# Performance work log

Hardware: AMD Instinct MI355X
Metric: run time of the kernel (lower is better)

The kernel has to match this reference:

```python
import jax, jax.numpy as jnp
import numpy as np

B = 2048
TT_IN = (16, 16, 16)    # prod = 4096
TT_OUT = (16, 16, 16)   # prod = 4096
BOND = (32, 32)
INIT_STD = 0.05  # keras 'random_normal' default stddev


def setup_inputs() -> dict:
    key = jax.random.key(0)
    k_x, k1, k2, k3 = jax.random.split(key, 4)
    x = jax.random.normal(k_x, (B, int(np.prod(TT_IN))), dtype=jnp.float32)
    core1 = jax.random.normal(k1, (TT_IN[0], TT_OUT[0], BOND[0]), dtype=jnp.float32) * INIT_STD
    core2 = jax.random.normal(k2, (TT_IN[1], TT_OUT[1], BOND[0], BOND[1]), dtype=jnp.float32) * INIT_STD
    core3 = jax.random.normal(k3, (TT_IN[2], TT_OUT[2], BOND[1]), dtype=jnp.float32) * INIT_STD
    bias = jnp.zeros(TT_OUT, dtype=jnp.float32)
    return {"x": x, "core1": core1, "core2": core2, "core3": core3, "bias": bias}


def reference(x, core1, core2, core3, bias):
    # x: [B, 4096] -> [B, x, y, z] tensor-train input modes
    xt = x.reshape((x.shape[0],) + TT_IN)
    # TT contraction: modes x,y,z contracted with cores; a,b,c are output
    # modes; p,q are bond indices (matches original einsum structure for
    # 3 cores: x[1,2,3], c1[1,4,7], c2[2,5,7,8], c3[3,6,8] -> [4,5,6]).
    out = jnp.einsum('nxyz,xap,ybpq,zcq->nabc', xt, core1, core2, core3,
                     optimize='optimal')
    out = out + bias  # bias broadcast over batch, shape TT_OUT
    out = out.reshape(x.shape[0], -1)  # [B, prod(TT_OUT)]
    return jax.nn.relu(out)
```

## Files before the change

kernel.cpp:

```cpp
#include <hip/hip_runtime.h>
#include <hip/hip_bf16.h>
#include <stdint.h>


typedef short bf16x8 __attribute__((ext_vector_type(8)));
typedef float f32x4  __attribute__((ext_vector_type(4)));

#define MB 2048
#define KD 4096
#define ND 4096
#define NT_K 64

__device__ __forceinline__ unsigned short f32_bf16(float f) {
  union { float f; uint32_t u; } v; v.f = f;
  return (unsigned short)((v.u + 0x7fffu + ((v.u >> 16) & 1u)) >> 16);
}
__device__ __forceinline__ float bf2f(unsigned short u) {
  union { uint32_t i; float f; } v; v.i = ((uint32_t)u) << 16; return v.f;
}

__global__ void k_conv(const float* __restrict__ x, unsigned short* __restrict__ xb) {
  int i = blockIdx.x * 256 + threadIdx.x;
  const float4* x4 = (const float4*)x;
  float4 a = x4[2*i];
  float4 b = x4[2*i+1];
  ushort4 lo, hi;
  lo.x = f32_bf16(a.x); lo.y = f32_bf16(a.y); lo.z = f32_bf16(a.z); lo.w = f32_bf16(a.w);
  hi.x = f32_bf16(b.x); hi.y = f32_bf16(b.y); hi.z = f32_bf16(b.z); hi.w = f32_bf16(b.w);
  ushort4* o = (ushort4*)xb;
  o[2*i]   = lo;
  o[2*i+1] = hi;
}

__global__ __launch_bounds__(256) void k_wt(const float* __restrict__ c1,
                                            const float* __restrict__ c2,
                                            const float* __restrict__ c3,
                                            unsigned short* __restrict__ Wt) {
  __shared__ unsigned short sh[17472];
  int ab = blockIdx.x;
  int t = threadIdx.x;
  int a = ab >> 4, b = ab & 15;
  unsigned short* c2s = sh;
  float* c1s = (float*)(sh + 16448);

  #pragma unroll
  for (int y = 0; y < 16; ++y) {
    float4 v = *(const float4*)(c2 + (size_t)(y*16 + b)*1024 + t*4);
    ushort4 s;
    s.x = f32_bf16(v.x); s.y = f32_bf16(v.y); s.z = f32_bf16(v.z); s.w = f32_bf16(v.w);
    *(ushort4*)(c2s + y*1028 + t*4) = s;
  }
  c1s[t]       = c1[((t>>5)*16 + a)*32 + (t&31)];
  c1s[t+256]   = c1[(((t>>5)+8)*16 + a)*32 + (t&31)];
  __syncthreads();

  int xx = t >> 4, yy = t & 15;
  const float* c1r = c1s + xx*32;
  const unsigned short* c2r = c2s + yy*1028;
  float acc[32];
  #pragma unroll
  for (int q = 0; q < 32; ++q) acc[q] = 0.f;
  #pragma unroll 8
  for (int p = 0; p < 32; ++p) {
    float w = c1r[p];
    #pragma unroll
    for (int j = 0; j < 8; ++j) {
      ushort4 v = *(const ushort4*)(c2r + p*32 + j*4);
      acc[4*j+0] = fmaf(w, bf2f(v.x), acc[4*j+0]);
      acc[4*j+1] = fmaf(w, bf2f(v.y), acc[4*j+1]);
      acc[4*j+2] = fmaf(w, bf2f(v.z), acc[4*j+2]);
      acc[4*j+3] = fmaf(w, bf2f(v.w), acc[4*j+3]);
    }
  }
  __syncthreads();

  unsigned short* T2s  = sh;
  unsigned short* c3ps = sh + 8192;

  #pragma unroll
  for (int j = 0; j < 8; ++j) {
    ushort4 s;
    s.x = f32_bf16(acc[4*j+0]); s.y = f32_bf16(acc[4*j+1]);
    s.z = f32_bf16(acc[4*j+2]); s.w = f32_bf16(acc[4*j+3]);
    *(ushort4*)(T2s + t*32 + j*4) = s;
  }
  #pragma unroll
  for (int r = 0; r < 8; ++r) {
    int i4 = t*8 + r;
    float4 v = *(const float4*)(c3 + (size_t)i4*4);
    int e = i4*4;
    int q = e & 31, zc = e >> 5;
    int z = zc >> 4, c = zc & 15;
    ushort4 s;
    s.x = f32_bf16(v.x); s.y = f32_bf16(v.y); s.z = f32_bf16(v.z); s.w = f32_bf16(v.w);
    *(ushort4*)(c3ps + (c*16 + z)*32 + q) = s;
  }
  __syncthreads();

  int wid = t >> 6, lane = t & 63, l15 = lane & 15, lg = lane >> 4;
  bf16x8 bfv[16];
  #pragma unroll
  for (int nt = 0; nt < 16; ++nt)
    bfv[nt] = *(const bf16x8*)(c3ps + (nt*16 + l15)*32 + lg*8);
  #pragma unroll
  for (int mi = 0; mi < 4; ++mi) {
    int mtile = wid*4 + mi;
    bf16x8 af = *(const bf16x8*)(T2s + (mtile*16 + l15)*32 + lg*8);
    #pragma unroll
    for (int nt = 0; nt < 16; ++nt) {
      f32x4 d = {0.f, 0.f, 0.f, 0.f};
      d = __builtin_amdgcn_mfma_f32_16x16x32_bf16(af, bfv[nt], d, 0, 0, 0);
      size_t jrow = (size_t)(ab*16 + nt) * ND;
      #pragma unroll
      for (int i = 0; i < 4; ++i) {
        int xy = mtile*16 + lg*4 + i;
        Wt[jrow + xy*16 + l15] = f32_bf16(d[i]);
      }
    }
  }
}

__device__ __forceinline__ void gload_lds16(const unsigned short* g, unsigned short* l) {
  __builtin_amdgcn_global_load_lds(
      (const __attribute__((address_space(1))) void*)g,
      (__attribute__((address_space(3))) void*)l, 16, 0, 0);
}

__global__ __launch_bounds__(512, 1) void k_gemm(const unsigned short* __restrict__ A,
                                                 const unsigned short* __restrict__ Bw,
                                                 const float* __restrict__ bias,
                                                 float* __restrict__ C) {
  __shared__ uint8_t sh[147456];
  unsigned short* As = (unsigned short*)sh;
  unsigned short* Bs = (unsigned short*)(sh + 49152);
  const int t = threadIdx.x;
  const int wid = t >> 6, lane = t & 63;
  const int l15 = lane & 15, lg = lane >> 4;
  const int m0 = blockIdx.y * 128;
  const int n0 = blockIdx.x * 256;
  const int wc  = wid & 3;
  const int kkw = wid >> 2;
  const int xr = l15 & 7;

  const int scol = (((t & 7) ^ ((t >> 3) & 7)) * 8);
  const int t8 = t * 8;
  const unsigned short* Ag = A  + (size_t)(m0 + (t >> 3))*KD + scol;
  const unsigned short* Bg = Bw + (size_t)(n0 + (t >> 3))*KD + scol;

#define STG_A(tk, buf, s) gload_lds16(Ag + (size_t)(s)*64*KD + (tk)*64, \
                                      As + (buf)*8192  + (s)*4096 + t8)
#define STG_B(tk, buf, s) gload_lds16(Bg + (size_t)(s)*64*KD + (tk)*64, \
                                      Bs + (buf)*16384 + (s)*4096 + t8)

  f32x4 acc[8][4];
  #pragma unroll
  for (int m = 0; m < 8; ++m)
    #pragma unroll
    for (int n = 0; n < 4; ++n)
      acc[m][n] = (f32x4){0.f, 0.f, 0.f, 0.f};

  STG_A(0,0,0); STG_A(0,0,1); STG_B(0,0,0); STG_B(0,0,1); STG_B(0,0,2); STG_B(0,0,3);
  STG_A(1,1,0); STG_A(1,1,1); STG_B(1,1,0); STG_B(1,1,1); STG_B(1,1,2); STG_B(1,1,3);
  asm volatile("s_waitcnt vmcnt(6)" ::: "memory");
  __builtin_amdgcn_s_barrier();

  const int pc8 = ((kkw*4 + lg) ^ xr) * 8;

  int cur = 0, stg = 2;
  for (int i = 0; i < NT_K; ++i) {
    const unsigned short* Ac = As + cur*8192;
    const unsigned short* Bc = Bs + cur*16384;
    bf16x8 aF[8], bF[4];
    #pragma unroll
    for (int m = 0; m < 8; ++m)
      aF[m] = *(const bf16x8*)(Ac + (m*16 + l15)*64 + pc8);
    #pragma unroll
    for (int n = 0; n < 4; ++n)
      bF[n] = *(const bf16x8*)(Bc + (wc*64 + n*16 + l15)*64 + pc8);
    if (i < NT_K - 2) {
      const int tk2 = i + 2;
      STG_A(tk2, stg, 0); STG_A(tk2, stg, 1);
      STG_B(tk2, stg, 0); STG_B(tk2, stg, 1); STG_B(tk2, stg, 2); STG_B(tk2, stg, 3);
    }
    asm volatile("s_waitcnt lgkmcnt(0)" ::: "memory");
    __builtin_amdgcn_sched_barrier(0);
    __builtin_amdgcn_s_setprio(1);
    #pragma unroll
    for (int m = 0; m < 8; ++m)
      #pragma unroll
      for (int n = 0; n < 4; ++n)
        acc[m][n] = __builtin_amdgcn_mfma_f32_16x16x32_bf16(aF[m], bF[n], acc[m][n], 0, 0, 0);
    __builtin_amdgcn_s_setprio(0);
    if (i < NT_K - 2)       { asm volatile("s_waitcnt vmcnt(6)" ::: "memory"); }
    else if (i == NT_K - 2) { asm volatile("s_waitcnt vmcnt(0)" ::: "memory"); }
    __builtin_amdgcn_s_barrier();
    cur = (cur == 2) ? 0 : cur + 1;
    stg = (stg == 2) ? 0 : stg + 1;
  }

  __syncthreads();
  float* mrg = (float*)sh;
  if (kkw == 1) {
    float* base = mrg + wc*8192;
    #pragma unroll
    for (int m = 0; m < 8; ++m)
      #pragma unroll
      for (int n = 0; n < 4; ++n)
        *(f32x4*)(base + ((m*4 + n)*64 + lane)*4) = acc[m][n];
  }
  __syncthreads();
  if (kkw == 0) {
    float* base = mrg + wc*8192;
    #pragma unroll
    for (int m = 0; m < 8; ++m) {
      int gr = m0 + m*16 + lg*4;
      #pragma unroll
      for (int n = 0; n < 4; ++n) {
        f32x4 o = *(const f32x4*)(base + ((m*4 + n)*64 + lane)*4);
        int gc = n0 + wc*64 + n*16 + l15;
        float bv = bias[gc];
        #pragma unroll
        for (int i = 0; i < 4; ++i) {
          float v = acc[m][n][i] + o[i] + bv;
          C[(size_t)(gr + i)*ND + gc] = v > 0.f ? v : 0.f;
        }
      }
    }
  }
#undef STG_A
#undef STG_B
}

extern "C" void kernel_launch(void* const* d_in, const int* in_sizes, int n_in,
                              void* d_out, int out_size, void* d_ws, size_t ws_size,
                              hipStream_t stream) {
  (void)in_sizes; (void)n_in; (void)out_size; (void)ws_size;
  const float* x    = (const float*)d_in[0];
  const float* c1   = (const float*)d_in[1];
  const float* c2   = (const float*)d_in[2];
  const float* c3   = (const float*)d_in[3];
  const float* bias = (const float*)d_in[4];
  float* out = (float*)d_out;

  uint8_t* ws = (uint8_t*)d_ws;
  unsigned short* xb = (unsigned short*)(ws);
  unsigned short* Wt = (unsigned short*)(ws + 16777216);

  k_conv<<<4096, 256, 0, stream>>>(x, xb);
  k_wt  <<<256,  256, 0, stream>>>(c1, c2, c3, Wt);
  k_gemm<<<dim3(ND/256, MB/128), 512, 0, stream>>>(xb, Wt, bias, out);
}
```

Measured before the change: 163.5 us.

## Software-pipeline GEMM with register double-buffered fragments and deeper LDS prefetch

Restructures the GEMM main loop to keep two sets of register fragments, so the LDS reads for the next K-tile are issued while MFMAs run on the current one. Global-to-LDS prefetch now runs three tiles ahead instead of two, and the loop is unrolled by two with the buffer rotation handled explicitly. The aim is to hide LDS read latency behind matrix math. In exchange it uses more registers per thread and a more intricate waitcnt and barrier schedule, which could introduce races or spills.

```diff
diff --git a/kernel.cpp b/kernel.cpp
--- a/kernel.cpp
+++ b/kernel.cpp
@@ -124,6 +124,28 @@
   __builtin_amdgcn_global_load_lds(
       (const __attribute__((address_space(1))) void*)g,
       (__attribute__((address_space(3))) void*)l, 16, 0, 0);
+}
+
+__device__ __forceinline__ void read_frags(const unsigned short* Ac, const unsigned short* Bc,
+                                           int wc, int l15, int pc8,
+                                           bf16x8 (&aF)[8], bf16x8 (&bF)[4]) {
+  #pragma unroll
+  for (int m = 0; m < 8; ++m)
+    aF[m] = *(const bf16x8*)(Ac + (m*16 + l15)*64 + pc8);
+  #pragma unroll
+  for (int n = 0; n < 4; ++n)
+    bF[n] = *(const bf16x8*)(Bc + (wc*64 + n*16 + l15)*64 + pc8);
+}
+
+__device__ __forceinline__ void do_mfma(const bf16x8 (&aF)[8], const bf16x8 (&bF)[4],
+                                        f32x4 (&acc)[8][4]) {
+  __builtin_amdgcn_s_setprio(1);
+  #pragma unroll
+  for (int m = 0; m < 8; ++m)
+    #pragma unroll
+    for (int n = 0; n < 4; ++n)
+      acc[m][n] = __builtin_amdgcn_mfma_f32_16x16x32_bf16(aF[m], bF[n], acc[m][n], 0, 0, 0);
+  __builtin_amdgcn_s_setprio(0);
 }
 
 __global__ __launch_bounds__(512, 1) void k_gemm(const unsigned short* __restrict__ A,
@@ -151,6 +173,8 @@
                                       As + (buf)*8192  + (s)*4096 + t8)
 #define STG_B(tk, buf, s) gload_lds16(Bg + (size_t)(s)*64*KD + (tk)*64, \
                                       Bs + (buf)*16384 + (s)*4096 + t8)
+#define STG_TILE(tk, buf) do { STG_A(tk, buf, 0); STG_A(tk, buf, 1); \
+    STG_B(tk, buf, 0); STG_B(tk, buf, 1); STG_B(tk, buf, 2); STG_B(tk, buf, 3); } while (0)
 
   f32x4 acc[8][4];
   #pragma unroll
@@ -159,43 +183,38 @@
     for (int n = 0; n < 4; ++n)
       acc[m][n] = (f32x4){0.f, 0.f, 0.f, 0.f};
 
-  STG_A(0,0,0); STG_A(0,0,1); STG_B(0,0,0); STG_B(0,0,1); STG_B(0,0,2); STG_B(0,0,3);
-  STG_A(1,1,0); STG_A(1,1,1); STG_B(1,1,0); STG_B(1,1,1); STG_B(1,1,2); STG_B(1,1,3);
-  asm volatile("s_waitcnt vmcnt(6)" ::: "memory");
+  const int pc8 = ((kkw*4 + lg) ^ xr) * 8;
+  bf16x8 frAa[8], frAb[4], frBa[8], frBb[4];
+
+  STG_TILE(0, 0); STG_TILE(1, 1); STG_TILE(2, 2);
+  asm volatile("s_waitcnt vmcnt(12)" ::: "memory");
   __builtin_amdgcn_s_barrier();
-
-  const int pc8 = ((kkw*4 + lg) ^ xr) * 8;
-
-  int cur = 0, stg = 2;
-  for (int i = 0; i < NT_K; ++i) {
-    const unsigned short* Ac = As + cur*8192;
-    const unsigned short* Bc = Bs + cur*16384;
-    bf16x8 aF[8], bF[4];
-    #pragma unroll
-    for (int m = 0; m < 8; ++m)
-      aF[m] = *(const bf16x8*)(Ac + (m*16 + l15)*64 + pc8);
-    #pragma unroll
-    for (int n = 0; n < 4; ++n)
-      bF[n] = *(const bf16x8*)(Bc + (wc*64 + n*16 + l15)*64 + pc8);
-    if (i < NT_K - 2) {
-      const int tk2 = i + 2;
-      STG_A(tk2, stg, 0); STG_A(tk2, stg, 1);
-      STG_B(tk2, stg, 0); STG_B(tk2, stg, 1); STG_B(tk2, stg, 2); STG_B(tk2, stg, 3);
-    }
+  read_frags(As, Bs, wc, l15, pc8, frAa, frAb);
+  asm volatile("s_waitcnt vmcnt(6) lgkmcnt(0)" ::: "memory");
+  __builtin_amdgcn_s_barrier();
+
+  int bi = 0;
+  for (int i = 0; i < NT_K; i += 2) {
+    const int bn1 = (bi + 1 < 3) ? bi + 1 : bi - 2;
+    const int bn2 = (bi + 2 < 3) ? bi + 2 : bi - 1;
+
+    if (i <= NT_K - 4) STG_TILE(i + 3, bi);
+    read_frags(As + bn1*8192, Bs + bn1*16384, wc, l15, pc8, frBa, frBb);
+    do_mfma(frAa, frAb, acc);
     asm volatile("s_waitcnt lgkmcnt(0)" ::: "memory");
-    __builtin_amdgcn_sched_barrier(0);
-    __builtin_amdgcn_s_setprio(1);
-    #pragma unroll
-    for (int m = 0; m < 8; ++m)
-      #pragma unroll
-      for (int n = 0; n < 4; ++n)
-        acc[m][n] = __builtin_amdgcn_mfma_f32_16x16x32_bf16(aF[m], bF[n], acc[m][n], 0, 0, 0);
-    __builtin_amdgcn_s_setprio(0);
-    if (i < NT_K - 2)       { asm volatile("s_waitcnt vmcnt(6)" ::: "memory"); }
-    else if (i == NT_K - 2) { asm volatile("s_waitcnt vmcnt(0)" ::: "memory"); }
+    if (i <= NT_K - 4) { asm volatile("s_waitcnt vmcnt(6)" ::: "memory"); }
     __builtin_amdgcn_s_barrier();
-    cur = (cur == 2) ? 0 : cur + 1;
-    stg = (stg == 2) ? 0 : stg + 1;
+
+    if (i + 1 <= NT_K - 5) STG_TILE(i + 4, bn1);
+    if (i + 1 <= NT_K - 2)
+      read_frags(As + bn2*8192, Bs + bn2*16384, wc, l15, pc8, frAa, frAb);
+    do_mfma(frBa, frBb, acc);
+    asm volatile("s_waitcnt lgkmcnt(0)" ::: "memory");
+    if (i + 1 <= NT_K - 4)      { asm volatile("s_waitcnt vmcnt(6)" ::: "memory"); }
+    else if (i + 1 == NT_K - 3) { asm volatile("s_waitcnt vmcnt(0)" ::: "memory"); }
+    if (i + 1 <= NT_K - 2) __builtin_amdgcn_s_barrier();
+
+    bi = bn2;
   }
 
   __syncthreads();
@@ -229,6 +248,7 @@
   }
 #undef STG_A
 #undef STG_B
+#undef STG_TILE
 }
 
 extern "C" void kernel_launch(void* const* d_in, const int* in_sizes, int n_in,
```

Result: no change. 163.5 us (+0.0%).
